# Kernel tuning notes

Hardware: AMD Instinct MI355X
Metric: run time of the kernel (lower is better)

The kernel has to match this reference:

```python
import jax, jax.numpy as jnp
import numpy as np

INF = 10000.0

# ---------- differentiable (jax) pieces ----------

def _embed(x, W1, b1, W2, b2):
    # nn.Sequential(Linear, Dropout(eval=identity), ReLU, Linear, ReLU)
    h = jax.nn.relu(x @ W1.T + b1)
    return jax.nn.relu(h @ W2.T + b2)


def _cdist(a, b):
    # batched euclidean cdist with zero-safe sqrt (matches torch.cdist values)
    sq = (jnp.sum(a * a, -1)[:, :, None]
          + jnp.sum(b * b, -1)[:, None, :]
          - 2.0 * jnp.einsum('bnd,bmd->bnm', a, b))
    sq = jnp.maximum(sq, 0.0)
    safe = jnp.where(sq > 0, sq, 1.0)
    return jnp.where(sq > 0, jnp.sqrt(safe), 0.0)


def _edit_costs(x_s, x_t, W1, b1, W2, b2, virtual, B, N):
    D = W2.shape[0]
    es = _embed(x_s, W1, b1, W2, b2).reshape(B, N, D)
    et = _embed(x_t, W1, b1, W2, b2).reshape(B, N, D)
    v = _embed(virtual[None, :], W1, b1, W2, b2)          # [1, D]
    vb = jnp.broadcast_to(v[None, :, :], (B, 1, D))
    es = jnp.concatenate([es, vb], axis=1)                # [B, N+1, D]
    et = jnp.concatenate([et, vb], axis=1)
    d = _cdist(es, et)                                    # [B, N+1, N+1]
    # per-pair normalization: d / sum(d) * (len_s * len_t)
    d = d / jnp.sum(d, axis=(1, 2), keepdims=True) * float(N * N)
    return d

# ---------- host-side LSAPE (replaces scipy.optimize.linear_sum_assignment) ----------

def _lsap(C):
    # Jonker-Volgenant / shortest augmenting path, square cost matrix.
    n = C.shape[0]
    u = np.zeros(n + 1)
    v = np.zeros(n + 1)
    p = np.zeros(n + 1, np.int64)    # p[j] = row matched to column j (1-indexed)
    way = np.zeros(n + 1, np.int64)
    for i in range(1, n + 1):
        p[0] = i
        j0 = 0
        minv = np.full(n + 1, np.inf)
        used = np.zeros(n + 1, bool)
        while True:
            used[j0] = True
            i0 = p[j0]
            free = np.nonzero(~used)[0]
            cur = C[i0 - 1, free - 1] - u[i0] - v[free]
            better = cur < minv[free]
            minv[free] = np.where(better, cur, minv[free])
            way[free] = np.where(better, j0, way[free])
            k = int(np.argmin(minv[free]))
            j1 = int(free[k])
            delta = minv[free][k]
            u[p[used]] += delta
            v[used] -= delta
            minv[free] -= delta
            j0 = j1
            if p[j0] == 0:
                break
        while j0 != 0:
            j1 = int(way[j0])
            p[j0] = p[j1]
            j0 = j1
    rows = p[1:] - 1
    cols = np.arange(n)
    return rows, cols


def _lsape(ec, n, m):
    # ec: (n+1, m+1) edit costs with virtual row/col; build (n+m)x(n+m) LSAPE matrix
    C = np.zeros((n + m, n + m))
    C[:n, :m] = ec[:n, :m]
    C[n:, :m] = INF
    C[:n, m:] = INF
    C[np.arange(n, n + m), np.arange(m)] = ec[n, :m]       # insertions
    C[np.arange(n), np.arange(m, m + n)] = ec[:n, m]       # deletions
    C[~np.isfinite(C)] = INF
    q, p = _lsap(C)
    A = np.zeros((n + 1, m + 1), np.int64)
    A[np.minimum(q, n), np.minimum(p, m)] = 1
    A[-1, -1] = 0
    return A

# ---------- harness ----------

def setup_inputs() -> dict:
    B, N, FIN, D = 16, 128, 512, 512
    key = jax.random.key(0)
    ks = jax.random.split(key, 7)
    s1 = 1.0 / np.sqrt(FIN)
    s2 = 1.0 / np.sqrt(D)
    return {
        'x_s': jax.random.normal(ks[0], (B * N, FIN), jnp.float32),
        'x_t': jax.random.normal(ks[1], (B * N, FIN), jnp.float32),
        'W1': jax.random.uniform(ks[2], (D, FIN), jnp.float32, -s1, s1),
        'b1': jax.random.uniform(ks[3], (D,), jnp.float32, -s1, s1),
        'W2': jax.random.uniform(ks[4], (D, D), jnp.float32, -s2, s2),
        'b2': jax.random.uniform(ks[5], (D,), jnp.float32, -s2, s2),
        'virtual': jax.random.uniform(ks[6], (FIN,), jnp.float32),
        'npairs': 16,
        'n_nodes': 128,
    }


def reference(x_s, x_t, W1, b1, W2, b2, virtual, npairs, n_nodes):
    B, N = int(npairs), int(n_nodes)
    edit = _edit_costs(x_s, x_t, W1, b1, W2, b2, virtual, B, N)  # [B, N+1, N+1]
    ec_np = np.asarray(jax.device_get(edit), np.float64)
    aligns = np.stack([_lsape(ec_np[i], N, N) for i in range(B)])
    A = jnp.asarray(aligns)                                      # [B, N+1, N+1] int
    geds = jnp.sum(A * edit, axis=(1, 2)) / float(2 * N)         # / (len_s + len_t)
    return (A, edit, geds)
```

## Files before the change

### kernel.cpp

```cpp
#include <hip/hip_runtime.h>

#define BATCH 16
#define NNODE 128
#define DIM 512
#define NP1 129
#define EDSZ (NP1 * NP1)
#define BIGF 3.0e38f

__global__ __launch_bounds__(256) void gemm2_nt_relu(
    const float* __restrict__ X0, const float* __restrict__ X1,
    const float* __restrict__ W, const float* __restrict__ bias,
    float* __restrict__ Y0, float* __restrict__ Y1,
    int M, int N, int K) {
  const float* X = blockIdx.z ? X1 : X0;
  float* Y = blockIdx.z ? Y1 : Y0;
  __shared__ float sA[32][68];
  __shared__ float sB[32][68];
  const int tid = threadIdx.x;
  const int m0 = blockIdx.x * 64;
  const int n0 = blockIdx.y * 64;
  const int tm = tid / 16, tn = tid % 16;
  const int lr = tid >> 2;
  const int lk8 = (tid & 3) * 8;
  float acc[4][4] = {};
  for (int k0 = 0; k0 < K; k0 += 32) {
    const float* xa = X + (size_t)(m0 + lr) * K + k0 + lk8;
    const float* wb = W + (size_t)(n0 + lr) * K + k0 + lk8;
    float4 a0 = *(const float4*)(xa);
    float4 a1 = *(const float4*)(xa + 4);
    float4 b0 = *(const float4*)(wb);
    float4 b1 = *(const float4*)(wb + 4);
    sA[lk8 + 0][lr] = a0.x; sA[lk8 + 1][lr] = a0.y;
    sA[lk8 + 2][lr] = a0.z; sA[lk8 + 3][lr] = a0.w;
    sA[lk8 + 4][lr] = a1.x; sA[lk8 + 5][lr] = a1.y;
    sA[lk8 + 6][lr] = a1.z; sA[lk8 + 7][lr] = a1.w;
    sB[lk8 + 0][lr] = b0.x; sB[lk8 + 1][lr] = b0.y;
    sB[lk8 + 2][lr] = b0.z; sB[lk8 + 3][lr] = b0.w;
    sB[lk8 + 4][lr] = b1.x; sB[lk8 + 5][lr] = b1.y;
    sB[lk8 + 6][lr] = b1.z; sB[lk8 + 7][lr] = b1.w;
    __syncthreads();
#pragma unroll
    for (int k = 0; k < 32; ++k) {
      const float4 a = *(const float4*)&sA[k][tm * 4];
      const float4 b = *(const float4*)&sB[k][tn * 4];
      acc[0][0] = fmaf(a.x, b.x, acc[0][0]);
      acc[0][1] = fmaf(a.x, b.y, acc[0][1]);
      acc[0][2] = fmaf(a.x, b.z, acc[0][2]);
      acc[0][3] = fmaf(a.x, b.w, acc[0][3]);
      acc[1][0] = fmaf(a.y, b.x, acc[1][0]);
      acc[1][1] = fmaf(a.y, b.y, acc[1][1]);
      acc[1][2] = fmaf(a.y, b.z, acc[1][2]);
      acc[1][3] = fmaf(a.y, b.w, acc[1][3]);
      acc[2][0] = fmaf(a.z, b.x, acc[2][0]);
      acc[2][1] = fmaf(a.z, b.y, acc[2][1]);
      acc[2][2] = fmaf(a.z, b.z, acc[2][2]);
      acc[2][3] = fmaf(a.z, b.w, acc[2][3]);
      acc[3][0] = fmaf(a.w, b.x, acc[3][0]);
      acc[3][1] = fmaf(a.w, b.y, acc[3][1]);
      acc[3][2] = fmaf(a.w, b.z, acc[3][2]);
      acc[3][3] = fmaf(a.w, b.w, acc[3][3]);
    }
    __syncthreads();
  }
#pragma unroll
  for (int i = 0; i < 4; ++i) {
    int m = m0 + tm * 4 + i;
#pragma unroll
    for (int j = 0; j < 4; ++j) {
      int n = n0 + tn * 4 + j;
      Y[(size_t)m * N + n] = fmaxf(acc[i][j] + bias[n], 0.f);
    }
  }
}

__global__ __launch_bounds__(256) void virt_embed(
    const float* __restrict__ x,
    const float* __restrict__ W1, const float* __restrict__ b1,
    const float* __restrict__ W2, const float* __restrict__ b2,
    float* __restrict__ e_v) {
  __shared__ float sx[DIM];
  __shared__ float sh[DIM];
  for (int k = threadIdx.x; k < DIM; k += 256) sx[k] = x[k];
  __syncthreads();
  for (int n = threadIdx.x; n < DIM; n += 256) {
    const float* w = W1 + (size_t)n * DIM;
    float s = 0.f;
    for (int k = 0; k < DIM; k += 4) {
      float4 wv = *(const float4*)(w + k);
      s = fmaf(sx[k + 0], wv.x, s);
      s = fmaf(sx[k + 1], wv.y, s);
      s = fmaf(sx[k + 2], wv.z, s);
      s = fmaf(sx[k + 3], wv.w, s);
    }
    sh[n] = fmaxf(s + b1[n], 0.f);
  }
  __syncthreads();
  for (int n = threadIdx.x; n < DIM; n += 256) {
    const float* w = W2 + (size_t)n * DIM;
    float s = 0.f;
    for (int k = 0; k < DIM; k += 4) {
      float4 wv = *(const float4*)(w + k);
      s = fmaf(sh[k + 0], wv.x, s);
      s = fmaf(sh[k + 1], wv.y, s);
      s = fmaf(sh[k + 2], wv.z, s);
      s = fmaf(sh[k + 3], wv.w, s);
    }
    e_v[n] = fmaxf(s + b2[n], 0.f);
  }
}

__global__ __launch_bounds__(256) void cdist_kernel(
    const float* __restrict__ es, const float* __restrict__ et,
    const float* __restrict__ ev, float* __restrict__ d) {
  const int b = blockIdx.z;
  const int i0 = blockIdx.x * 32;
  const int j0 = blockIdx.y * 32;
  __shared__ float sA[32][33];
  __shared__ float sB[32][33];
  const int tid = threadIdx.x;
  const int ty = tid / 16, tx = tid % 16;
  const int lr = tid / 8;
  const int lk4 = (tid % 8) * 4;
  const int gi = i0 + lr;
  const int gj = j0 + lr;
  const float* pa = (gi < NNODE) ? (es + ((size_t)b * NNODE + gi) * DIM) : ev;
  const float* pb = (gj < NNODE) ? (et + ((size_t)b * NNODE + gj) * DIM) : ev;
  float acc[2][2] = {};
  for (int k0 = 0; k0 < DIM; k0 += 32) {
    float4 av = *(const float4*)(pa + k0 + lk4);
    float4 bv = *(const float4*)(pb + k0 + lk4);
    sA[lr][lk4 + 0] = av.x; sA[lr][lk4 + 1] = av.y;
    sA[lr][lk4 + 2] = av.z; sA[lr][lk4 + 3] = av.w;
    sB[lr][lk4 + 0] = bv.x; sB[lr][lk4 + 1] = bv.y;
    sB[lr][lk4 + 2] = bv.z; sB[lr][lk4 + 3] = bv.w;
    __syncthreads();
#pragma unroll 8
    for (int k = 0; k < 32; ++k) {
      float a0 = sA[ty * 2 + 0][k], a1 = sA[ty * 2 + 1][k];
      float b0 = sB[tx * 2 + 0][k], b1 = sB[tx * 2 + 1][k];
      float d00 = a0 - b0, d01 = a0 - b1, d10 = a1 - b0, d11 = a1 - b1;
      acc[0][0] = fmaf(d00, d00, acc[0][0]);
      acc[0][1] = fmaf(d01, d01, acc[0][1]);
      acc[1][0] = fmaf(d10, d10, acc[1][0]);
      acc[1][1] = fmaf(d11, d11, acc[1][1]);
    }
    __syncthreads();
  }
#pragma unroll
  for (int i = 0; i < 2; ++i) {
    int gi2 = i0 + ty * 2 + i;
#pragma unroll
    for (int j = 0; j < 2; ++j) {
      int gj2 = j0 + tx * 2 + j;
      if (gi2 < NP1 && gj2 < NP1)
        d[(size_t)b * EDSZ + gi2 * NP1 + gj2] = sqrtf(acc[i][j]);
    }
  }
}

__global__ __launch_bounds__(256) void batch_sum(
    const float* __restrict__ d, float* __restrict__ sums) {
  const int b = blockIdx.x;
  double s = 0.0;
  for (int idx = threadIdx.x; idx < EDSZ; idx += 256)
    s += (double)d[(size_t)b * EDSZ + idx];
  __shared__ double red[256];
  red[threadIdx.x] = s;
  __syncthreads();
  for (int off = 128; off; off >>= 1) {
    if (threadIdx.x < off) red[threadIdx.x] += red[threadIdx.x + off];
    __syncthreads();
  }
  if (threadIdx.x == 0) sums[b] = (float)red[0];
}

__global__ __launch_bounds__(256) void normalize_kernel(
    const float* __restrict__ d, const float* __restrict__ sums,
    float* __restrict__ edit) {
  int idx = blockIdx.x * 256 + threadIdx.x;
  if (idx < BATCH * EDSZ) {
    int b = idx / EDSZ;
    edit[idx] = d[idx] / sums[b] * (float)(NNODE * NNODE);
  }
}

__device__ __forceinline__ unsigned key_of(float m, int col) {
  return (__float_as_uint(m) & 0xFFFFFF80u) | (unsigned)col;
}

template <int CTRL>
__device__ __forceinline__ unsigned dpp_umin_step(unsigned x) {
  const unsigned o = (unsigned)__builtin_amdgcn_update_dpp(
      (int)0xFFFFFFFFu, (int)x, CTRL, 0xf, 0xf, false);
  return o < x ? o : x;
}

__device__ __forceinline__ unsigned wave_umin_key(unsigned x) {
  x = dpp_umin_step<0x111>(x);
  x = dpp_umin_step<0x112>(x);
  x = dpp_umin_step<0x114>(x);
  x = dpp_umin_step<0x118>(x);
  x = dpp_umin_step<0x142>(x);
  x = dpp_umin_step<0x143>(x);
  return (unsigned)__builtin_amdgcn_readlane((int)x, 63);
}

template <int CTRL>
__device__ __forceinline__ void dpp_umin2_step(unsigned& m1, unsigned& m2) {
  const unsigned o1 = (unsigned)__builtin_amdgcn_update_dpp(
      (int)0xFFFFFFFFu, (int)m1, CTRL, 0xf, 0xf, false);
  const unsigned o2 = (unsigned)__builtin_amdgcn_update_dpp(
      (int)0xFFFFFFFFu, (int)m2, CTRL, 0xf, 0xf, false);
  const unsigned lo = m1 < o1 ? m1 : o1;
  const unsigned hi = m1 < o1 ? o1 : m1;
  const unsigned yo = m2 < o2 ? m2 : o2;
  m1 = lo;
  m2 = hi < yo ? hi : yo;
}

__device__ __forceinline__ void wave_umin2_key(unsigned a, unsigned b,
                                               unsigned& k1, unsigned& k2) {
  unsigned m1 = a < b ? a : b;
  unsigned m2 = a < b ? b : a;
  dpp_umin2_step<0x111>(m1, m2);
  dpp_umin2_step<0x112>(m1, m2);
  dpp_umin2_step<0x114>(m1, m2);
  dpp_umin2_step<0x118>(m1, m2);
  dpp_umin2_step<0x142>(m1, m2);
  dpp_umin2_step<0x143>(m1, m2);
  k1 = (unsigned)__builtin_amdgcn_readlane((int)m1, 63);
  k2 = (unsigned)__builtin_amdgcn_readlane((int)m2, 63);
}

__device__ __forceinline__ float fsel2(float a0, float a1, int s) {
  return (s == 0) ? a0 : a1;
}
__device__ __forceinline__ int isel2(int a0, int a1, int s) {
  return (s == 0) ? a0 : a1;
}
__device__ __forceinline__ float readlane_f32(float x, int lane) {
  return __uint_as_float(
      (unsigned)__builtin_amdgcn_readlane((int)__float_as_uint(x), lane));
}

__global__ __launch_bounds__(64) void lsap_kernel(
    const float* __restrict__ edit, float* __restrict__ Aout,
    float* __restrict__ geds) {
  const int b = blockIdx.x;
  const float* ec = edit + (size_t)b * EDSZ;
  float* A = Aout + (size_t)b * EDSZ;
  const int lane = threadIdx.x;
  const int cbase = lane * 2;

  __shared__ float D[NNODE * NNODE];

  for (int idx = lane; idx < NNODE * NNODE; idx += 64) {
    const int i = idx >> 7, j = idx & 127;
    const float sub = ec[i * NP1 + j];
    const float di = ec[i * NP1 + NNODE] + ec[NNODE * NP1 + j];
    D[idx] = fminf(sub, di);
  }
  for (int idx = lane; idx < EDSZ; idx += 64) A[idx] = 0.f;
  __syncthreads();

  float u0 = 0.f, u1 = 0.f;
  float v0 = 0.f, v1 = 0.f;
  float m0, m1;
  int w0 = 0, w1 = 0;
  int p0 = 0, p1 = 0;
  int x0 = 0, x1 = 0;

  int y0 = 0, y1 = 0;
  {
    float c0 = BIGF, c1 = BIGF;
    for (int r = 0; r < NNODE; ++r) {
      const float2 f = *(const float2*)&D[r * NNODE + cbase];
      if (f.x < c0) { c0 = f.x; y0 = r; }
      if (f.y < c1) { c1 = f.y; y1 = r; }
    }
    v0 = c0; v1 = c1;
  }

  unsigned long long ra0 = 0, ra1 = 0;
  for (int j = 0; j < NNODE; ++j) {
    const int jl = j >> 1, jq = j & 1;
    const int i1 = __builtin_amdgcn_readlane(isel2(y0, y1, jq), jl);
    const int bit = i1 & 63;
    const unsigned long long msk = (i1 < 64) ? ra0 : ra1;
    if (!((msk >> bit) & 1ull)) {
      if (i1 < 64) ra0 |= 1ull << bit; else ra1 |= 1ull << bit;
      if (lane == jl) {
        if (jq == 0) p0 = i1 + 1;
        else p1 = i1 + 1;
      }
      if (lane == (i1 >> 1)) {
        if ((i1 & 1) == 0) x0 = j + 1;
        else x1 = j + 1;
      }
    }
  }

  for (int ii = 0; ii < NNODE; ++ii) {
    const int xj = __builtin_amdgcn_readlane(isel2(x0, x1, ii & 1), ii >> 1);
    if (xj == 0) continue;
    const int j1 = xj - 1;
    const float2 f = *(const float2*)&D[ii * NNODE + cbase];
    float r0 = fmaxf(f.x - v0, 0.f);
    float r1 = fmaxf(f.y - v1, 0.f);
    if (cbase + 0 == j1) r0 = BIGF;
    if (cbase + 1 == j1) r1 = BIGF;
    const unsigned ka = key_of(r0, cbase + 0);
    const unsigned kb = key_of(r1, cbase + 1);
    const unsigned kmin = wave_umin_key(ka < kb ? ka : kb);
    const int jm = (int)(kmin & 127u);
    const float umin = readlane_f32(fsel2(r0, r1, jm & 1), jm >> 1);
    if (lane == (j1 >> 1)) {
      if ((j1 & 1) == 0) v0 -= umin; else v1 -= umin;
    }
    if (lane == (ii >> 1)) {
      if ((ii & 1) == 0) u0 = umin; else u1 = umin;
    }
  }

  {
    const int nfree0 =
        NNODE - __builtin_popcountll(ra0) - __builtin_popcountll(ra1);
    const int budget = 2 * nfree0 + 8;
    for (int step = 0; step < budget; ++step) {
      const unsigned long long fm0 = ~ra0, fm1 = ~ra1;
      int i;
      if (fm0) i = __builtin_ctzll(fm0);
      else if (fm1) i = 64 + __builtin_ctzll(fm1);
      else break;

      const float2 f = *(const float2*)&D[i * NNODE + cbase];
      const float r0 = fmaxf(f.x - v0, 0.f);
      const float r1 = fmaxf(f.y - v1, 0.f);
      unsigned k1, k2;
      wave_umin2_key(key_of(r0, cbase + 0), key_of(r1, cbase + 1), k1, k2);
      const int j1 = (int)(k1 & 127u), j2 = (int)(k2 & 127u);
      const float u1v = readlane_f32(fsel2(r0, r1, j1 & 1), j1 >> 1);
      const float u2v = readlane_f32(fsel2(r0, r1, j2 & 1), j2 >> 1);

      int jt = j1;
      int i1 = __builtin_amdgcn_readlane(isel2(p0, p1, j1 & 1), j1 >> 1);
      if (u1v < u2v) {
        const float dv = u2v - u1v;
        if (lane == (j1 >> 1)) {
          if ((j1 & 1) == 0) v0 -= dv; else v1 -= dv;
        }
      } else if (i1 != 0) {
        jt = j2;
        i1 = __builtin_amdgcn_readlane(isel2(p0, p1, j2 & 1), j2 >> 1);
      }
      if (lane == (jt >> 1)) {
        if ((jt & 1) == 0) p0 = i + 1; else p1 = i + 1;
      }
      if (lane == (i >> 1)) {
        if ((i & 1) == 0) u0 = u2v; else u1 = u2v;
      }
      if (i < 64) ra0 |= 1ull << i; else ra1 |= 1ull << (i - 64);
      if (i1 != 0) {
        const int rr = i1 - 1;
        if (rr < 64) ra0 &= ~(1ull << rr); else ra1 &= ~(1ull << (rr - 64));
        if (lane == (rr >> 1)) {
          if ((rr & 1) == 0) u0 = 0.f; else u1 = 0.f;
        }
      }
    }
  }

  for (int ii = 0; ii < NNODE; ++ii) {
    const unsigned long long amsk = (ii < 64) ? ra0 : ra1;
    if ((amsk >> (ii & 63)) & 1ull) continue;
    const int i = ii + 1;

    unsigned cused = 0, rused = 0;
    m0 = m1 = BIGF;
    int j0 = 0;
    int i0 = i;
    for (int guard = 0; guard <= NNODE; ++guard) {
      if (j0 > 0 && lane == ((j0 - 1) >> 1)) {
        if (((j0 - 1) & 1) == 0) { cused |= 1u; m0 = BIGF; }
        else { cused |= 2u; m1 = BIGF; }
      }
      if (lane == ((i0 - 1) >> 1)) rused |= 1u << ((i0 - 1) & 1);

      const float u_i0 = readlane_f32(fsel2(u0, u1, (i0 - 1) & 1), (i0 - 1) >> 1);

      const float2 f = *(const float2*)&D[(i0 - 1) * NNODE + cbase];

      const bool f0 = !(cused & 1u), f1 = !(cused & 2u);
      {
        float cur = fmaxf(f.x - u_i0 - v0, 0.f);
        bool up = f0 && (cur < m0);
        m0 = up ? cur : m0; w0 = up ? j0 : w0;
      }
      {
        float cur = fmaxf(f.y - u_i0 - v1, 0.f);
        bool up = f1 && (cur < m1);
        m1 = up ? cur : m1; w1 = up ? j0 : w1;
      }

      const unsigned ka = key_of(m0, cbase + 0);
      const unsigned kb = key_of(m1, cbase + 1);
      const unsigned kmin = wave_umin_key(ka < kb ? ka : kb);
      const int jcol = (int)(kmin & 127u);
      const float delta = readlane_f32(fsel2(m0, m1, jcol & 1), jcol >> 1);
      const int j1 = jcol + 1;

      if (!f0) v0 -= delta; else m0 = fmaxf(m0 - delta, 0.f);
      if (!f1) v1 -= delta; else m1 = fmaxf(m1 - delta, 0.f);
      if (rused & 1u) u0 += delta;
      if (rused & 2u) u1 += delta;

      const int pj1 = __builtin_amdgcn_readlane(
          isel2(p0, p1, (j1 - 1) & 1), (j1 - 1) >> 1);
      j0 = j1;
      if (pj1 == 0) break;
      i0 = pj1;
    }

    int jc = j0;
    while (jc != 0) {
      const int cl = (jc - 1) >> 1, cq = (jc - 1) & 1;
      const int jp = __builtin_amdgcn_readlane(isel2(w0, w1, cq), cl);
      const int js = (jp == 0) ? 1 : jp;
      const int pvr = __builtin_amdgcn_readlane(
          isel2(p0, p1, (js - 1) & 1), (js - 1) >> 1);
      const int pv = (jp == 0) ? i : pvr;
      if (lane == cl) {
        if (cq == 0) p0 = pv;
        else p1 = pv;
      }
      jc = jp;
    }
  }

  double contrib = 0.0;
  {
    const int pr[2] = {p0, p1};
#pragma unroll
    for (int q = 0; q < 2; ++q) {
      const int j = cbase + q;
      const int i = pr[q] - 1;
      const float sub = ec[i * NP1 + j];
      const float di = ec[i * NP1 + NNODE] + ec[NNODE * NP1 + j];
      if (sub < di) {
        A[i * NP1 + j] = 1.f;
        contrib += (double)sub;
      } else {
        A[i * NP1 + NNODE] = 1.f;
        A[NNODE * NP1 + j] = 1.f;
        contrib += (double)di;
      }
    }
  }
#pragma unroll
  for (int off = 32; off; off >>= 1) contrib += __shfl_xor(contrib, off);
  if (lane == 0) geds[b] = (float)(contrib / 256.0);
}

extern "C" void kernel_launch(void* const* d_in, const int* in_sizes, int n_in,
                              void* d_out, int out_size, void* d_ws, size_t ws_size,
                              hipStream_t stream) {
  const float* x_s  = (const float*)d_in[0];
  const float* x_t  = (const float*)d_in[1];
  const float* W1   = (const float*)d_in[2];
  const float* b1   = (const float*)d_in[3];
  const float* W2   = (const float*)d_in[4];
  const float* b2   = (const float*)d_in[5];
  const float* virt = (const float*)d_in[6];

  const int M = BATCH * NNODE;

  float* ws    = (float*)d_ws;
  float* h_s   = ws;
  float* h_t   = h_s + (size_t)M * DIM;
  float* e_s   = h_t + (size_t)M * DIM;
  float* e_t   = e_s + (size_t)M * DIM;
  float* e_v   = e_t + (size_t)M * DIM;
  float* d_raw = e_v + DIM;
  float* sums  = d_raw + (size_t)BATCH * EDSZ;

  float* Aout = (float*)d_out;
  float* edit = Aout + (size_t)BATCH * EDSZ;
  float* geds = edit + (size_t)BATCH * EDSZ;

  dim3 gblk(M / 64, DIM / 64, 2);
  virt_embed<<<1, 256, 0, stream>>>(virt, W1, b1, W2, b2, e_v);
  gemm2_nt_relu<<<gblk, 256, 0, stream>>>(x_s, x_t, W1, b1, h_s, h_t, M, DIM, DIM);
  gemm2_nt_relu<<<gblk, 256, 0, stream>>>(h_s, h_t, W2, b2, e_s, e_t, M, DIM, DIM);

  cdist_kernel<<<dim3(5, 5, BATCH), 256, 0, stream>>>(e_s, e_t, e_v, d_raw);
  batch_sum<<<BATCH, 256, 0, stream>>>(d_raw, sums);
  normalize_kernel<<<(BATCH * EDSZ + 255) / 256, 256, 0, stream>>>(d_raw, sums, edit);
  lsap_kernel<<<BATCH, 64, 0, stream>>>(edit, Aout, geds);
}
```

Baseline: 823.6 us.

## Solve two LSAP instances per wavefront using half-wave lanes

The LSAP solver now handles two batch items per 64-lane wavefront. Each half-wave owns 32 lanes with 4 columns per lane, and the DPP reductions are split so both halves find their minimum in lockstep. The reduced cost matrix D is built by a separate parallel kernel, and the A output is zeroed with a memset instead of inside the serial kernel. One matrix is staged in LDS and the other is read from global memory. The augmenting-reduction phase is removed, and both instances run the full shortest-path loop in lockstep, so the slower instance sets the pace. This halves the number of blocks to 8, which uses fewer CUs but aims to cut per-instance serial latency.

```diff
diff --git a/kernel.cpp b/kernel.cpp
--- a/kernel.cpp
+++ b/kernel.cpp
@@ -5,6 +5,7 @@
 #define DIM 512
 #define NP1 129
 #define EDSZ (NP1 * NP1)
+#define LSN 256
 #define BIGF 3.0e38f
 
 __global__ __launch_bounds__(256) void gemm2_nt_relu(
@@ -184,6 +185,18 @@
   }
 }
 
+__global__ __launch_bounds__(256) void build_D(
+    const float* __restrict__ edit, float* __restrict__ Dg) {
+  int idx = blockIdx.x * 256 + threadIdx.x;
+  if (idx < BATCH * NNODE * NNODE) {
+    const int b = idx >> 14;
+    const int rc = idx & 16383;
+    const int i = rc >> 7, j = rc & 127;
+    const float* ec = edit + (size_t)b * EDSZ;
+    Dg[idx] = fminf(ec[i * NP1 + j], ec[i * NP1 + NNODE] + ec[NNODE * NP1 + j]);
+  }
+}
+
 __device__ __forceinline__ unsigned key_of(float m, int col) {
   return (__float_as_uint(m) & 0xFFFFFF80u) | (unsigned)col;
 }
@@ -195,254 +208,288 @@
   return o < x ? o : x;
 }
 
-__device__ __forceinline__ unsigned wave_umin_key(unsigned x) {
+__device__ __forceinline__ void half_umin_key(unsigned x, unsigned& kA,
+                                              unsigned& kB) {
   x = dpp_umin_step<0x111>(x);
   x = dpp_umin_step<0x112>(x);
   x = dpp_umin_step<0x114>(x);
   x = dpp_umin_step<0x118>(x);
   x = dpp_umin_step<0x142>(x);
-  x = dpp_umin_step<0x143>(x);
-  return (unsigned)__builtin_amdgcn_readlane((int)x, 63);
-}
-
-template <int CTRL>
-__device__ __forceinline__ void dpp_umin2_step(unsigned& m1, unsigned& m2) {
-  const unsigned o1 = (unsigned)__builtin_amdgcn_update_dpp(
-      (int)0xFFFFFFFFu, (int)m1, CTRL, 0xf, 0xf, false);
-  const unsigned o2 = (unsigned)__builtin_amdgcn_update_dpp(
-      (int)0xFFFFFFFFu, (int)m2, CTRL, 0xf, 0xf, false);
-  const unsigned lo = m1 < o1 ? m1 : o1;
-  const unsigned hi = m1 < o1 ? o1 : m1;
-  const unsigned yo = m2 < o2 ? m2 : o2;
-  m1 = lo;
-  m2 = hi < yo ? hi : yo;
-}
-
-__device__ __forceinline__ void wave_umin2_key(unsigned a, unsigned b,
-                                               unsigned& k1, unsigned& k2) {
-  unsigned m1 = a < b ? a : b;
-  unsigned m2 = a < b ? b : a;
-  dpp_umin2_step<0x111>(m1, m2);
-  dpp_umin2_step<0x112>(m1, m2);
-  dpp_umin2_step<0x114>(m1, m2);
-  dpp_umin2_step<0x118>(m1, m2);
-  dpp_umin2_step<0x142>(m1, m2);
-  dpp_umin2_step<0x143>(m1, m2);
-  k1 = (unsigned)__builtin_amdgcn_readlane((int)m1, 63);
-  k2 = (unsigned)__builtin_amdgcn_readlane((int)m2, 63);
-}
-
-__device__ __forceinline__ float fsel2(float a0, float a1, int s) {
-  return (s == 0) ? a0 : a1;
-}
-__device__ __forceinline__ int isel2(int a0, int a1, int s) {
-  return (s == 0) ? a0 : a1;
+  kA = (unsigned)__builtin_amdgcn_readlane((int)x, 31);
+  kB = (unsigned)__builtin_amdgcn_readlane((int)x, 63);
+}
+
+__device__ __forceinline__ float fsel4(float a0, float a1, float a2, float a3,
+                                       int s) {
+  return (s == 0) ? a0 : (s == 1) ? a1 : (s == 2) ? a2 : a3;
+}
+__device__ __forceinline__ int isel4(int a0, int a1, int a2, int a3, int s) {
+  return (s == 0) ? a0 : (s == 1) ? a1 : (s == 2) ? a2 : a3;
 }
 __device__ __forceinline__ float readlane_f32(float x, int lane) {
   return __uint_as_float(
       (unsigned)__builtin_amdgcn_readlane((int)__float_as_uint(x), lane));
 }
-
-__global__ __launch_bounds__(64) void lsap_kernel(
-    const float* __restrict__ edit, float* __restrict__ Aout,
-    float* __restrict__ geds) {
-  const int b = blockIdx.x;
-  const float* ec = edit + (size_t)b * EDSZ;
-  float* A = Aout + (size_t)b * EDSZ;
+__device__ __forceinline__ float rl2_f32(float sel, int laneA, int laneB,
+                                         int h) {
+  const float a = readlane_f32(sel, laneA);
+  const float b = readlane_f32(sel, laneB);
+  return h ? b : a;
+}
+
+__global__ __launch_bounds__(64) void lsap_hw(
+    const float* __restrict__ edit, const float* __restrict__ Dg,
+    float* __restrict__ Aout, float* __restrict__ geds) {
+  const int bid = blockIdx.x;
   const int lane = threadIdx.x;
-  const int cbase = lane * 2;
-
-  __shared__ float D[NNODE * NNODE];
-
-  for (int idx = lane; idx < NNODE * NNODE; idx += 64) {
-    const int i = idx >> 7, j = idx & 127;
-    const float sub = ec[i * NP1 + j];
-    const float di = ec[i * NP1 + NNODE] + ec[NNODE * NP1 + j];
-    D[idx] = fminf(sub, di);
-  }
-  for (int idx = lane; idx < EDSZ; idx += 64) A[idx] = 0.f;
+  const int h = lane >> 5;
+  const int t = lane & 31;
+  const int cb = t * 4;
+
+  const float* DgA = Dg + (size_t)(2 * bid + 0) * (NNODE * NNODE);
+  const float* DgB = Dg + (size_t)(2 * bid + 1) * (NNODE * NNODE);
+
+  __shared__ float DL[NNODE * NNODE];
+  for (int idx = lane * 4; idx < NNODE * NNODE; idx += 256)
+    *(float4*)&DL[idx] = *(const float4*)&DgA[idx];
   __syncthreads();
 
-  float u0 = 0.f, u1 = 0.f;
-  float v0 = 0.f, v1 = 0.f;
-  float m0, m1;
-  int w0 = 0, w1 = 0;
-  int p0 = 0, p1 = 0;
-  int x0 = 0, x1 = 0;
-
-  int y0 = 0, y1 = 0;
+  auto fetch_row = [&](int rv) -> float4 {
+    const float4 a = *(const float4*)&DL[rv * NNODE + cb];
+    const float4 b = *(const float4*)&DgB[(size_t)rv * NNODE + cb];
+    float4 r;
+    r.x = h ? b.x : a.x; r.y = h ? b.y : a.y;
+    r.z = h ? b.z : a.z; r.w = h ? b.w : a.w;
+    return r;
+  };
+
+  float u0 = 0.f, u1 = 0.f, u2 = 0.f, u3 = 0.f;
+  float v0, v1, v2, v3, m0, m1, m2, m3;
+  int w0 = 0, w1 = 0, w2 = 0, w3 = 0;
+  int p0 = 0, p1 = 0, p2 = 0, p3 = 0;
+  int x0 = 0, x1 = 0, x2 = 0, x3 = 0;
+
+  int y0 = 0, y1 = 0, y2 = 0, y3 = 0;
   {
-    float c0 = BIGF, c1 = BIGF;
+    float c0 = BIGF, c1 = BIGF, c2 = BIGF, c3 = BIGF;
     for (int r = 0; r < NNODE; ++r) {
-      const float2 f = *(const float2*)&D[r * NNODE + cbase];
+      const float4 f = fetch_row(r);
       if (f.x < c0) { c0 = f.x; y0 = r; }
       if (f.y < c1) { c1 = f.y; y1 = r; }
-    }
-    v0 = c0; v1 = c1;
-  }
-
-  unsigned long long ra0 = 0, ra1 = 0;
+      if (f.z < c2) { c2 = f.z; y2 = r; }
+      if (f.w < c3) { c3 = f.w; y3 = r; }
+    }
+    v0 = c0; v1 = c1; v2 = c2; v3 = c3;
+  }
+
+  unsigned long long raA0 = 0, raA1 = 0, raB0 = 0, raB1 = 0;
   for (int j = 0; j < NNODE; ++j) {
-    const int jl = j >> 1, jq = j & 1;
-    const int i1 = __builtin_amdgcn_readlane(isel2(y0, y1, jq), jl);
-    const int bit = i1 & 63;
-    const unsigned long long msk = (i1 < 64) ? ra0 : ra1;
-    if (!((msk >> bit) & 1ull)) {
-      if (i1 < 64) ra0 |= 1ull << bit; else ra1 |= 1ull << bit;
-      if (lane == jl) {
-        if (jq == 0) p0 = i1 + 1;
-        else p1 = i1 + 1;
-      }
-      if (lane == (i1 >> 1)) {
-        if ((i1 & 1) == 0) x0 = j + 1;
-        else x1 = j + 1;
+    const int jl = j >> 2, jq = j & 3;
+    const int sely = isel4(y0, y1, y2, y3, jq);
+    const int iA = __builtin_amdgcn_readlane(sely, jl);
+    const int iB = __builtin_amdgcn_readlane(sely, 32 + jl);
+    {
+      const unsigned long long msk = (iA < 64) ? raA0 : raA1;
+      if (!((msk >> (iA & 63)) & 1ull)) {
+        if (iA < 64) raA0 |= 1ull << iA; else raA1 |= 1ull << (iA - 64);
+        if (h == 0 && t == jl) {
+          if (jq == 0) p0 = iA + 1; else if (jq == 1) p1 = iA + 1;
+          else if (jq == 2) p2 = iA + 1; else p3 = iA + 1;
+        }
+        if (h == 0 && t == (iA >> 2)) {
+          const int q = iA & 3;
+          if (q == 0) x0 = j + 1; else if (q == 1) x1 = j + 1;
+          else if (q == 2) x2 = j + 1; else x3 = j + 1;
+        }
+      }
+    }
+    {
+      const unsigned long long msk = (iB < 64) ? raB0 : raB1;
+      if (!((msk >> (iB & 63)) & 1ull)) {
+        if (iB < 64) raB0 |= 1ull << iB; else raB1 |= 1ull << (iB - 64);
+        if (h == 1 && t == jl) {
+          if (jq == 0) p0 = iB + 1; else if (jq == 1) p1 = iB + 1;
+          else if (jq == 2) p2 = iB + 1; else p3 = iB + 1;
+        }
+        if (h == 1 && t == (iB >> 2)) {
+          const int q = iB & 3;
+          if (q == 0) x0 = j + 1; else if (q == 1) x1 = j + 1;
+          else if (q == 2) x2 = j + 1; else x3 = j + 1;
+        }
       }
     }
   }
 
   for (int ii = 0; ii < NNODE; ++ii) {
-    const int xj = __builtin_amdgcn_readlane(isel2(x0, x1, ii & 1), ii >> 1);
-    if (xj == 0) continue;
-    const int j1 = xj - 1;
-    const float2 f = *(const float2*)&D[ii * NNODE + cbase];
+    const int selx = isel4(x0, x1, x2, x3, ii & 3);
+    const int xjA = __builtin_amdgcn_readlane(selx, ii >> 2);
+    const int xjB = __builtin_amdgcn_readlane(selx, 32 + (ii >> 2));
+    const float4 f = fetch_row(ii);
+    const int xjv = h ? xjB : xjA;
+    const int j1v = xjv - 1;
     float r0 = fmaxf(f.x - v0, 0.f);
     float r1 = fmaxf(f.y - v1, 0.f);
-    if (cbase + 0 == j1) r0 = BIGF;
-    if (cbase + 1 == j1) r1 = BIGF;
-    const unsigned ka = key_of(r0, cbase + 0);
-    const unsigned kb = key_of(r1, cbase + 1);
-    const unsigned kmin = wave_umin_key(ka < kb ? ka : kb);
-    const int jm = (int)(kmin & 127u);
-    const float umin = readlane_f32(fsel2(r0, r1, jm & 1), jm >> 1);
-    if (lane == (j1 >> 1)) {
-      if ((j1 & 1) == 0) v0 -= umin; else v1 -= umin;
-    }
-    if (lane == (ii >> 1)) {
-      if ((ii & 1) == 0) u0 = umin; else u1 = umin;
-    }
-  }
-
-  {
-    const int nfree0 =
-        NNODE - __builtin_popcountll(ra0) - __builtin_popcountll(ra1);
-    const int budget = 2 * nfree0 + 8;
-    for (int step = 0; step < budget; ++step) {
-      const unsigned long long fm0 = ~ra0, fm1 = ~ra1;
-      int i;
-      if (fm0) i = __builtin_ctzll(fm0);
-      else if (fm1) i = 64 + __builtin_ctzll(fm1);
-      else break;
-
-      const float2 f = *(const float2*)&D[i * NNODE + cbase];
-      const float r0 = fmaxf(f.x - v0, 0.f);
-      const float r1 = fmaxf(f.y - v1, 0.f);
-      unsigned k1, k2;
-      wave_umin2_key(key_of(r0, cbase + 0), key_of(r1, cbase + 1), k1, k2);
-      const int j1 = (int)(k1 & 127u), j2 = (int)(k2 & 127u);
-      const float u1v = readlane_f32(fsel2(r0, r1, j1 & 1), j1 >> 1);
-      const float u2v = readlane_f32(fsel2(r0, r1, j2 & 1), j2 >> 1);
-
-      int jt = j1;
-      int i1 = __builtin_amdgcn_readlane(isel2(p0, p1, j1 & 1), j1 >> 1);
-      if (u1v < u2v) {
-        const float dv = u2v - u1v;
-        if (lane == (j1 >> 1)) {
-          if ((j1 & 1) == 0) v0 -= dv; else v1 -= dv;
-        }
-      } else if (i1 != 0) {
-        jt = j2;
-        i1 = __builtin_amdgcn_readlane(isel2(p0, p1, j2 & 1), j2 >> 1);
-      }
-      if (lane == (jt >> 1)) {
-        if ((jt & 1) == 0) p0 = i + 1; else p1 = i + 1;
-      }
-      if (lane == (i >> 1)) {
-        if ((i & 1) == 0) u0 = u2v; else u1 = u2v;
-      }
-      if (i < 64) ra0 |= 1ull << i; else ra1 |= 1ull << (i - 64);
-      if (i1 != 0) {
-        const int rr = i1 - 1;
-        if (rr < 64) ra0 &= ~(1ull << rr); else ra1 &= ~(1ull << (rr - 64));
-        if (lane == (rr >> 1)) {
-          if ((rr & 1) == 0) u0 = 0.f; else u1 = 0.f;
-        }
-      }
-    }
-  }
-
-  for (int ii = 0; ii < NNODE; ++ii) {
-    const unsigned long long amsk = (ii < 64) ? ra0 : ra1;
-    if ((amsk >> (ii & 63)) & 1ull) continue;
-    const int i = ii + 1;
+    float r2 = fmaxf(f.z - v2, 0.f);
+    float r3 = fmaxf(f.w - v3, 0.f);
+    if (cb + 0 == j1v) r0 = BIGF;
+    if (cb + 1 == j1v) r1 = BIGF;
+    if (cb + 2 == j1v) r2 = BIGF;
+    if (cb + 3 == j1v) r3 = BIGF;
+    const unsigned kk =
+        min(min(key_of(r0, cb + 0), key_of(r1, cb + 1)),
+            min(key_of(r2, cb + 2), key_of(r3, cb + 3)));
+    unsigned kA, kB;
+    half_umin_key(kk, kA, kB);
+    const int jmA = (int)(kA & 127u), jmB = (int)(kB & 127u);
+    const int jmv = h ? jmB : jmA;
+    const float selr = fsel4(r0, r1, r2, r3, jmv & 3);
+    const float uminv = rl2_f32(selr, jmA >> 2, 32 + (jmB >> 2), h);
+    if (xjv != 0) {
+      if (t == (j1v >> 2)) {
+        const int q = j1v & 3;
+        if (q == 0) v0 -= uminv; else if (q == 1) v1 -= uminv;
+        else if (q == 2) v2 -= uminv; else v3 -= uminv;
+      }
+      if (t == (ii >> 2)) {
+        const int q = ii & 3;
+        if (q == 0) u0 = uminv; else if (q == 1) u1 = uminv;
+        else if (q == 2) u2 = uminv; else u3 = uminv;
+      }
+    }
+  }
+
+  for (int outer = 0; outer < NNODE; ++outer) {
+    const unsigned long long fA0 = ~raA0, fA1 = ~raA1;
+    const unsigned long long fB0 = ~raB0, fB1 = ~raB1;
+    const bool actA = (fA0 | fA1) != 0ull;
+    const bool actB = (fB0 | fB1) != 0ull;
+    if (!actA && !actB) break;
+    const int iA = fA0 ? (__builtin_ctzll(fA0) + 1)
+                       : (fA1 ? (64 + __builtin_ctzll(fA1) + 1) : 1);
+    const int iB = fB0 ? (__builtin_ctzll(fB0) + 1)
+                       : (fB1 ? (64 + __builtin_ctzll(fB1) + 1) : 1);
 
     unsigned cused = 0, rused = 0;
-    m0 = m1 = BIGF;
-    int j0 = 0;
-    int i0 = i;
-    for (int guard = 0; guard <= NNODE; ++guard) {
-      if (j0 > 0 && lane == ((j0 - 1) >> 1)) {
-        if (((j0 - 1) & 1) == 0) { cused |= 1u; m0 = BIGF; }
-        else { cused |= 2u; m1 = BIGF; }
-      }
-      if (lane == ((i0 - 1) >> 1)) rused |= 1u << ((i0 - 1) & 1);
-
-      const float u_i0 = readlane_f32(fsel2(u0, u1, (i0 - 1) & 1), (i0 - 1) >> 1);
-
-      const float2 f = *(const float2*)&D[(i0 - 1) * NNODE + cbase];
+    m0 = m1 = m2 = m3 = BIGF;
+    int j0A = 0, j0B = 0, i0A = iA, i0B = iB;
+    bool pA = actA, pB = actB;
+
+    for (int g = 0; g <= LSN && (pA || pB); ++g) {
+      const int i0v = h ? i0B : i0A;
+      const int j0v = h ? j0B : j0A;
+      const bool pv = h ? pB : pA;
+
+      if (pv && j0v > 0 && t == ((j0v - 1) >> 2)) {
+        const int q = (j0v - 1) & 3;
+        cused |= 1u << q;
+        if (q == 0) m0 = BIGF; else if (q == 1) m1 = BIGF;
+        else if (q == 2) m2 = BIGF; else m3 = BIGF;
+      }
+      if (pv && t == ((i0v - 1) >> 2)) rused |= 1u << ((i0v - 1) & 3);
+
+      const float uc = fsel4(u0, u1, u2, u3, (i0v - 1) & 3);
+      const float u_i0 =
+          rl2_f32(uc, (i0A - 1) >> 2, 32 + ((i0B - 1) >> 2), h);
+
+      const float4 f = fetch_row(i0v - 1);
 
       const bool f0 = !(cused & 1u), f1 = !(cused & 2u);
+      const bool f2 = !(cused & 4u), f3 = !(cused & 8u);
       {
         float cur = fmaxf(f.x - u_i0 - v0, 0.f);
-        bool up = f0 && (cur < m0);
-        m0 = up ? cur : m0; w0 = up ? j0 : w0;
+        bool up = pv && f0 && (cur < m0);
+        m0 = up ? cur : m0; w0 = up ? j0v : w0;
       }
       {
         float cur = fmaxf(f.y - u_i0 - v1, 0.f);
-        bool up = f1 && (cur < m1);
-        m1 = up ? cur : m1; w1 = up ? j0 : w1;
-      }
-
-      const unsigned ka = key_of(m0, cbase + 0);
-      const unsigned kb = key_of(m1, cbase + 1);
-      const unsigned kmin = wave_umin_key(ka < kb ? ka : kb);
-      const int jcol = (int)(kmin & 127u);
-      const float delta = readlane_f32(fsel2(m0, m1, jcol & 1), jcol >> 1);
-      const int j1 = jcol + 1;
-
-      if (!f0) v0 -= delta; else m0 = fmaxf(m0 - delta, 0.f);
-      if (!f1) v1 -= delta; else m1 = fmaxf(m1 - delta, 0.f);
-      if (rused & 1u) u0 += delta;
-      if (rused & 2u) u1 += delta;
-
-      const int pj1 = __builtin_amdgcn_readlane(
-          isel2(p0, p1, (j1 - 1) & 1), (j1 - 1) >> 1);
-      j0 = j1;
-      if (pj1 == 0) break;
-      i0 = pj1;
-    }
-
-    int jc = j0;
-    while (jc != 0) {
-      const int cl = (jc - 1) >> 1, cq = (jc - 1) & 1;
-      const int jp = __builtin_amdgcn_readlane(isel2(w0, w1, cq), cl);
-      const int js = (jp == 0) ? 1 : jp;
-      const int pvr = __builtin_amdgcn_readlane(
-          isel2(p0, p1, (js - 1) & 1), (js - 1) >> 1);
-      const int pv = (jp == 0) ? i : pvr;
-      if (lane == cl) {
-        if (cq == 0) p0 = pv;
-        else p1 = pv;
-      }
-      jc = jp;
-    }
-  }
-
-  double contrib = 0.0;
+        bool up = pv && f1 && (cur < m1);
+        m1 = up ? cur : m1; w1 = up ? j0v : w1;
+      }
+      {
+        float cur = fmaxf(f.z - u_i0 - v2, 0.f);
+        bool up = pv && f2 && (cur < m2);
+        m2 = up ? cur : m2; w2 = up ? j0v : w2;
+      }
+      {
+        float cur = fmaxf(f.w - u_i0 - v3, 0.f);
+        bool up = pv && f3 && (cur < m3);
+        m3 = up ? cur : m3; w3 = up ? j0v : w3;
+      }
+
+      const unsigned kk =
+          min(min(key_of(m0, cb + 0), key_of(m1, cb + 1)),
+              min(key_of(m2, cb + 2), key_of(m3, cb + 3)));
+      unsigned kA, kB;
+      half_umin_key(kk, kA, kB);
+      const int jA = (int)(kA & 127u), jB = (int)(kB & 127u);
+      const int jv = h ? jB : jA;
+      const float dsel = fsel4(m0, m1, m2, m3, jv & 3);
+      const float delta = rl2_f32(dsel, jA >> 2, 32 + (jB >> 2), h);
+
+      if (pv) {
+        if (!f0) v0 -= delta; else m0 = fmaxf(m0 - delta, 0.f);
+        if (!f1) v1 -= delta; else m1 = fmaxf(m1 - delta, 0.f);
+        if (!f2) v2 -= delta; else m2 = fmaxf(m2 - delta, 0.f);
+        if (!f3) v3 -= delta; else m3 = fmaxf(m3 - delta, 0.f);
+        if (rused & 1u) u0 += delta;
+        if (rused & 2u) u1 += delta;
+        if (rused & 4u) u2 += delta;
+        if (rused & 8u) u3 += delta;
+      }
+
+      const int psel = isel4(p0, p1, p2, p3, jv & 3);
+      const int pj1A = __builtin_amdgcn_readlane(psel, jA >> 2);
+      const int pj1B = __builtin_amdgcn_readlane(psel, 32 + (jB >> 2));
+      if (pA) { j0A = jA + 1; if (pj1A == 0) pA = false; else i0A = pj1A; }
+      if (pB) { j0B = jB + 1; if (pj1B == 0) pB = false; else i0B = pj1B; }
+    }
+
+    int jcA = actA ? j0A : 0, jcB = actB ? j0B : 0;
+    for (int g = 0; g <= LSN && (jcA || jcB); ++g) {
+      const int jcv = h ? jcB : jcA;
+      const int jcs = (jcv == 0) ? 1 : jcv;
+      const int wsel = isel4(w0, w1, w2, w3, (jcs - 1) & 3);
+      const int jsA = (jcA == 0) ? 1 : jcA;
+      const int jsB = (jcB == 0) ? 1 : jcB;
+      const int jpA = __builtin_amdgcn_readlane(wsel, (jsA - 1) >> 2);
+      const int jpB = __builtin_amdgcn_readlane(wsel, 32 + ((jsB - 1) >> 2));
+      const int jpv = h ? jpB : jpA;
+      const int jps = (jpv == 0) ? 1 : jpv;
+      const int psel2 = isel4(p0, p1, p2, p3, (jps - 1) & 3);
+      const int jqA = (jpA == 0) ? 1 : jpA;
+      const int jqB = (jpB == 0) ? 1 : jpB;
+      const int pvrA = __builtin_amdgcn_readlane(psel2, (jqA - 1) >> 2);
+      const int pvrB = __builtin_amdgcn_readlane(psel2, 32 + ((jqB - 1) >> 2));
+      const int pvA = (jpA == 0) ? iA : pvrA;
+      const int pvB = (jpB == 0) ? iB : pvrB;
+      const int pvv = h ? pvB : pvA;
+      if (jcv != 0 && t == ((jcv - 1) >> 2)) {
+        const int q = (jcv - 1) & 3;
+        if (q == 0) p0 = pvv; else if (q == 1) p1 = pvv;
+        else if (q == 2) p2 = pvv; else p3 = pvv;
+      }
+      jcA = (jcA == 0) ? 0 : jpA;
+      jcB = (jcB == 0) ? 0 : jpB;
+    }
+    if (actA) {
+      const int r = iA - 1;
+      if (r < 64) raA0 |= 1ull << r; else raA1 |= 1ull << (r - 64);
+    }
+    if (actB) {
+      const int r = iB - 1;
+      if (r < 64) raB0 |= 1ull << r; else raB1 |= 1ull << (r - 64);
+    }
+  }
+
   {
-    const int pr[2] = {p0, p1};
-#pragma unroll
-    for (int q = 0; q < 2; ++q) {
-      const int j = cbase + q;
+    const int b = 2 * bid + h;
+    const float* ec = edit + (size_t)b * EDSZ;
+    float* A = Aout + (size_t)b * EDSZ;
+    double contrib = 0.0;
+    const int pr[4] = {p0, p1, p2, p3};
+#pragma unroll
+    for (int q = 0; q < 4; ++q) {
+      const int j = cb + q;
       const int i = pr[q] - 1;
       const float sub = ec[i * NP1 + j];
       const float di = ec[i * NP1 + NNODE] + ec[NNODE * NP1 + j];
@@ -455,10 +502,10 @@
         contrib += (double)di;
       }
     }
-  }
-#pragma unroll
-  for (int off = 32; off; off >>= 1) contrib += __shfl_xor(contrib, off);
-  if (lane == 0) geds[b] = (float)(contrib / 256.0);
+#pragma unroll
+    for (int off = 16; off; off >>= 1) contrib += __shfl_xor(contrib, off);
+    if (t == 0) geds[b] = (float)(contrib / 256.0);
+  }
 }
 
 extern "C" void kernel_launch(void* const* d_in, const int* in_sizes, int n_in,
@@ -482,10 +529,13 @@
   float* e_v   = e_t + (size_t)M * DIM;
   float* d_raw = e_v + DIM;
   float* sums  = d_raw + (size_t)BATCH * EDSZ;
+  float* Dg    = sums + 16;
 
   float* Aout = (float*)d_out;
   float* edit = Aout + (size_t)BATCH * EDSZ;
   float* geds = edit + (size_t)BATCH * EDSZ;
+
+  hipMemsetAsync(Aout, 0, (size_t)BATCH * EDSZ * sizeof(float), stream);
 
   dim3 gblk(M / 64, DIM / 64, 2);
   virt_embed<<<1, 256, 0, stream>>>(virt, W1, b1, W2, b2, e_v);
@@ -495,5 +545,6 @@
   cdist_kernel<<<dim3(5, 5, BATCH), 256, 0, stream>>>(e_s, e_t, e_v, d_raw);
   batch_sum<<<BATCH, 256, 0, stream>>>(d_raw, sums);
   normalize_kernel<<<(BATCH * EDSZ + 255) / 256, 256, 0, stream>>>(d_raw, sums, edit);
-  lsap_kernel<<<BATCH, 64, 0, stream>>>(edit, Aout, geds);
-}
+  build_D<<<(BATCH * NNODE * NNODE + 255) / 256, 256, 0, stream>>>(edit, Dg);
+  lsap_hw<<<BATCH / 2, 64, 0, stream>>>(edit, Dg, Aout, geds);
+}
```

New measurement: 1.975 ms. 2.4x slower.
